# Kernel optimization log

Measured on AMD Instinct MI355X. Metric: run time of the kernel, lower is better.

## Reference

```python
import jax, jax.numpy as jnp
import numpy as np
from jax import lax

B = 8
INPUT_DIM = 2048
N_ENC = 2
VOCAB = 32000
EMBED = 512
HIDDEN = 512
MAX_LEN = 32
TEMP = 1.0


def setup_inputs() -> dict:
    key = jax.random.key(0)
    ks = jax.random.split(key, 12)
    s = 0.02
    inp = {
        "x": jax.random.normal(ks[0], (B, INPUT_DIM), jnp.float32),
        # encoder: N_ENC tanh layers input_dim->input_dim (stacked), then linear input_dim->embed
        "enc_w": jax.random.normal(ks[1], (N_ENC, INPUT_DIM, INPUT_DIM), jnp.float32) * s,
        "enc_b": jnp.zeros((N_ENC, INPUT_DIM), jnp.float32),
        "out_w": jax.random.normal(ks[2], (EMBED, INPUT_DIM), jnp.float32) * s,  # nn.Linear weight [out,in]
        "out_b": jnp.zeros((EMBED,), jnp.float32),
        # embeddings.weight: [vocab, hidden]; hidden_to_output = its transpose
        "emb_out": jax.random.normal(ks[3], (VOCAB, HIDDEN), jnp.float32) * s,
        # RelaxedEmbedding weight: [vocab, embed]
        "emb_in": jax.random.normal(ks[4], (VOCAB, EMBED), jnp.float32) * s,
        "prev_hidden0": jnp.zeros((HIDDEN,), jnp.float32),  # nn.Parameter init zeros
        # torch GRUCell params: weight_ih [3H, E], weight_hh [3H, H], biases [3H]
        "w_ih": jax.random.normal(ks[5], (3 * HIDDEN, EMBED), jnp.float32) * s,
        "b_ih": jnp.zeros((3 * HIDDEN,), jnp.float32),
        "w_hh": jax.random.normal(ks[6], (3 * HIDDEN, HIDDEN), jnp.float32) * s,
        "b_hh": jnp.zeros((3 * HIDDEN,), jnp.float32),
        # pre-sampled gumbel noise, one per step: [T, B, V]
        "gumbel": jax.random.gumbel(ks[7], (MAX_LEN, B, VOCAB), jnp.float32),
    }
    return inp


def reference(x, enc_w, enc_b, out_w, out_b, emb_out, emb_in, prev_hidden0,
              w_ih, b_ih, w_hh, b_hh, gumbel):
    # encoder MLP
    h = x
    for i in range(N_ENC):
        h = jnp.tanh(h @ enc_w[i].T + enc_b[i])
    img_feats = h @ out_w.T + out_b  # [B, EMBED]

    h0 = jnp.broadcast_to(prev_hidden0, (x.shape[0], HIDDEN))
    e0 = jnp.zeros_like(img_feats)  # sos_embedding * img_feats == 0

    def step(carry, g_t):
        h_prev, e_t = carry
        gi = e_t @ w_ih.T + b_ih      # [B, 3H]
        gh = h_prev @ w_hh.T + b_hh   # [B, 3H]
        i_r, i_z, i_n = jnp.split(gi, 3, axis=-1)
        h_r, h_z, h_n = jnp.split(gh, 3, axis=-1)
        r = jax.nn.sigmoid(i_r + h_r)
        z = jax.nn.sigmoid(i_z + h_z)
        n = jnp.tanh(i_n + r * h_n)
        h_t = (1.0 - z) * n + z * h_prev               # GRUCell
        logits = h_t @ emb_out.T                        # [B, V]
        x_t = jax.nn.softmax((logits + g_t) / TEMP, axis=-1)  # relaxed one-hot (training, no ST)
        e_next = (x_t @ emb_in) * img_feats             # RelaxedEmbedding * img_feats
        return (h_t, e_next), x_t

    _, seq = lax.scan(step, (h0, e0), gumbel)  # [T, B, V]
    return jnp.transpose(seq, (1, 0, 2))        # [B, T, V]
```

## Files before the change

### kernel.cpp

```cpp
#include <hip/hip_runtime.h>
#include <math.h>

constexpr int DIM = 2048, EMB = 512, HID = 512, VOC = 32000, TLEN = 32, G3 = 1536;
constexpr int NB = 256;
constexpr int NT = 256;
constexpr int ROWS = 125;
constexpr unsigned MAGIC = 0x13579BDFu;

constexpr size_t W_H1  = 0;
constexpr size_t W_H2  = W_H1 + 8 * 2048;
constexpr size_t W_IMG = W_H2 + 8 * 2048;
constexpr size_t W_GI  = W_IMG + 8 * 512;
constexpr size_t W_GH  = W_GI + 8 * 1536;
constexpr size_t W_SB  = W_GH + 8 * 1536;
constexpr size_t W_RS  = W_SB + (size_t)TLEN * 4096;
constexpr size_t W_AF  = W_RS + TLEN * 8;
constexpr size_t W_GF  = W_AF + 256 * 16;
constexpr size_t W_HF  = W_GF + 64 * 16;
constexpr size_t W_CNT = W_HF + 64 * 16;
constexpr size_t W_RDY = W_CNT + 32;
constexpr int FLAG_WORDS = 256 * 16 + 64 * 16 * 2 + 32;

__device__ __forceinline__ float dot4(float4 a, float4 b) {
  return a.x * b.x + a.y * b.y + a.z * b.z + a.w * b.w;
}
__device__ __forceinline__ float4 fma4(float4 acc, float s, float4 v) {
  acc.x += s * v.x; acc.y += s * v.y; acc.z += s * v.z; acc.w += s * v.w; return acc;
}
__device__ __forceinline__ float4 add4(float4 a, float4 b) {
  a.x += b.x; a.y += b.y; a.z += b.z; a.w += b.w; return a;
}
__device__ __forceinline__ float sigm(float x) { return 1.0f / (1.0f + __expf(-x)); }
__device__ __forceinline__ float selLane8(const float pb[8]) {
  int lane = threadIdx.x & 63;
  float r = 0.0f;
#pragma unroll
  for (int b = 0; b < 8; b++) r = (lane == b) ? pb[b] : r;
  return r;
}

__device__ __forceinline__ void stC(float* p, float v) {
  __hip_atomic_store(p, v, __ATOMIC_RELAXED, __HIP_MEMORY_SCOPE_AGENT);
}
__device__ __forceinline__ float ldC(const float* p) {
  return __hip_atomic_load(p, __ATOMIC_RELAXED, __HIP_MEMORY_SCOPE_AGENT);
}
__device__ __forceinline__ void vdrain() {
  asm volatile("s_waitcnt vmcnt(0)" ::: "memory");
}

template <int KLEN>
__device__ __forceinline__ void rowdot8(const float* __restrict__ wrow,
                                        const float* __restrict__ xsrc, float pb[8]) {
  constexpr int PER = KLEN / 64;
  constexpr int NF4 = PER / 4;
  int lane = threadIdx.x & 63;
  int k0 = lane * PER;
  const float4* w4 = (const float4*)(wrow + k0);
  float4 wv[NF4];
#pragma unroll
  for (int i = 0; i < NF4; i++) wv[i] = w4[i];
#pragma unroll
  for (int b = 0; b < 8; b++) {
    const float4* x4 = (const float4*)(xsrc + b * KLEN + k0);
    float s = 0.0f;
#pragma unroll
    for (int i = 0; i < NF4; i++) s += dot4(x4[i], wv[i]);
    pb[b] = s;
  }
#pragma unroll
  for (int m = 1; m < 64; m <<= 1) {
#pragma unroll
    for (int b = 0; b < 8; b++) pb[b] += __shfl_xor(pb[b], m, 64);
  }
}

__device__ __forceinline__ void postSlotF(unsigned* slot, unsigned val) {
  __syncthreads();
  if (threadIdx.x == 0) {
    __threadfence();
    __hip_atomic_store(slot, val, __ATOMIC_RELEASE, __HIP_MEMORY_SCOPE_AGENT);
  }
}
__device__ __forceinline__ void pollSlotsF(const unsigned* slots, int n, unsigned tgt) {
  int tid = threadIdx.x;
  if (tid < n) {
    const unsigned* p = slots + (size_t)tid * 16;
    while (__hip_atomic_load(p, __ATOMIC_RELAXED, __HIP_MEMORY_SCOPE_AGENT) < tgt)
      __builtin_amdgcn_s_sleep(1);
  }
  __syncthreads();
  __threadfence();
}

__device__ __forceinline__ void postSlotQ(unsigned* slot, unsigned val) {
  vdrain();
  __syncthreads();
  if (threadIdx.x == 0)
    __hip_atomic_store(slot, val, __ATOMIC_RELAXED, __HIP_MEMORY_SCOPE_AGENT);
}
__device__ __forceinline__ void pollOne(const unsigned* p, unsigned tgt) {
  if (threadIdx.x == 0) {
    while (__hip_atomic_load(p, __ATOMIC_RELAXED, __HIP_MEMORY_SCOPE_AGENT) < tgt)
      __builtin_amdgcn_s_sleep(1);
  }
  __syncthreads();
}

__device__ __forceinline__ void vocabRow(int r, float4 a0, float4 a1, float4 i0, float4 i1,
                                         const float4 hf[8][2], float4 ea[8][2],
                                         float sums[8], float* __restrict__ p_lds,
                                         const float* __restrict__ gum_lds) {
  int lane = threadIdx.x & 63;
  float pb[8];
#pragma unroll
  for (int b = 0; b < 8; b++) pb[b] = dot4(hf[b][0], a0) + dot4(hf[b][1], a1);
#pragma unroll
  for (int m = 1; m < 64; m <<= 1) {
#pragma unroll
    for (int b = 0; b < 8; b++) pb[b] += __shfl_xor(pb[b], m, 64);
  }
#pragma unroll
  for (int b = 0; b < 8; b++) {
    pb[b] = __expf(pb[b] + gum_lds[r * 8 + b]);
    sums[b] += pb[b];
  }
  if (lane == 0) {
    *(float4*)&p_lds[r * 8] = make_float4(pb[0], pb[1], pb[2], pb[3]);
    *(float4*)&p_lds[r * 8 + 4] = make_float4(pb[4], pb[5], pb[6], pb[7]);
  }
#pragma unroll
  for (int b = 0; b < 8; b++) {
    ea[b][0] = fma4(ea[b][0], pb[b], i0);
    ea[b][1] = fma4(ea[b][1], pb[b], i1);
  }
}

__global__ void __launch_bounds__(NT, 1)
InformedRnnSenderFixedLengthGS_48704929136907_kernel(
    const float* __restrict__ x, const float* __restrict__ enc_w,
    const float* __restrict__ enc_b, const float* __restrict__ out_w,
    const float* __restrict__ out_b, const float* __restrict__ emb_out,
    const float* __restrict__ emb_in, const float* __restrict__ ph,
    const float* __restrict__ w_ih, const float* __restrict__ b_ih,
    const float* __restrict__ w_hh, const float* __restrict__ b_hh,
    const float* __restrict__ gum, float* __restrict__ out, float* __restrict__ ws) {
  const int tid = threadIdx.x, blk = blockIdx.x;
  const int lane = tid & 63, wave = tid >> 6;

  float* h1 = ws + W_H1;
  float* h2 = ws + W_H2;
  float* img = ws + W_IMG;
  float* giU = ws + W_GI;
  float* gh = ws + W_GH;
  float* sbufU = ws + W_SB;
  float* rs_acc = ws + W_RS;
  unsigned* aflag = (unsigned*)(ws + W_AF);
  unsigned* gflag = (unsigned*)(ws + W_GF);
  unsigned* hflag = (unsigned*)(ws + W_HF);
  unsigned* cnt_gru = (unsigned*)(ws + W_CNT);
  unsigned* cnt_e = (unsigned*)(ws + W_CNT) + 16;
  unsigned* ready = (unsigned*)(ws + W_RDY);

  __shared__ float h_lds[4096];
  __shared__ float red_e[4096];
  __shared__ float p_lds[ROWS * 8];
  __shared__ float gum_lds[ROWS * 8];
  __shared__ float bih_lds[G3];
  __shared__ float red_rs[32];
  __shared__ float inv_lds[8];

  if (blk == 0) {
    for (int i = tid; i < FLAG_WORDS; i += NT) aflag[i] = 0u;
    __syncthreads();
    if (tid == 0) {
      __threadfence();
      __hip_atomic_store(ready, MAGIC, __ATOMIC_RELEASE, __HIP_MEMORY_SCOPE_AGENT);
    }
  }
  if (tid == 0) {
    while (__hip_atomic_load(ready, __ATOMIC_ACQUIRE, __HIP_MEMORY_SCOPE_AGENT) != MAGIC)
      __builtin_amdgcn_s_sleep(1);
  }
  __syncthreads();
  __threadfence();

#pragma unroll
  for (int rr = 0; rr < 2; rr++) {
    int o = blk * 8 + wave * 2 + rr;
    float pb[8];
    rowdot8<2048>(enc_w + (size_t)o * DIM, x, pb);
    float eb = enc_b[o];
#pragma unroll
    for (int b = 0; b < 8; b++) pb[b] = tanhf(pb[b] + eb);
    float myv = selLane8(pb);
    if (lane < 8) h1[lane * DIM + o] = myv;
  }
  postSlotF(&aflag[blk * 16], 1u);
  pollSlotsF(aflag, 256, 1u);

#pragma unroll
  for (int rr = 0; rr < 2; rr++) {
    int o = blk * 8 + wave * 2 + rr;
    float pb[8];
    rowdot8<2048>(enc_w + (size_t)DIM * DIM + (size_t)o * DIM, h1, pb);
    float eb = enc_b[DIM + o];
#pragma unroll
    for (int b = 0; b < 8; b++) pb[b] = tanhf(pb[b] + eb);
    float myv = selLane8(pb);
    if (lane < 8) h2[lane * DIM + o] = myv;
  }
  postSlotF(&aflag[blk * 16], 2u);
  pollSlotsF(aflag, 256, 2u);

  if (blk < 64) {
#pragma unroll
    for (int rr = 0; rr < 2; rr++) {
      int o = blk * 8 + wave * 2 + rr;
      float pb[8];
      rowdot8<2048>(out_w + (size_t)o * DIM, h2, pb);
      float ob = out_b[o];
#pragma unroll
      for (int b = 0; b < 8; b++) pb[b] += ob;
      float myv = selLane8(pb);
      if (lane < 8) img[lane * EMB + o] = myv;
    }
  } else if (blk < 128) {
    int local = blk - 64;
    int kk = lane * 8;
    float4 p0 = *(const float4*)(ph + kk);
    float4 p1 = *(const float4*)(ph + kk + 4);
    for (int r = 0; r < 6; r++) {
      int j = local * 24 + wave * 6 + r;
      const float4* w4 = (const float4*)(w_hh + (size_t)j * HID + kk);
      float s = dot4(p0, w4[0]) + dot4(p1, w4[1]);
#pragma unroll
      for (int m = 1; m < 64; m <<= 1) s += __shfl_xor(s, m, 64);
      float val = s + b_hh[j];
      if (lane < 8) gh[lane * G3 + j] = val;
    }
  } else if (blk < 192) {
    int local = blk - 128;
    for (int r = 0; r < 6; r++) {
      int j = local * 24 + wave * 6 + r;
      if (lane < 8) giU[lane * G3 + j] = 0.0f;
    }
  }
  for (int i = tid; i < 4096; i += NT) h_lds[i] = ph[i & 511];
  for (int i = tid; i < G3; i += NT) bih_lds[i] = b_ih[i];
  if (tid < 8) inv_lds[tid] = 1.0f;
  __syncthreads();
  postSlotF(&aflag[blk * 16], 3u);
  pollSlotsF(aflag, 256, 3u);

  const int v0 = blk * ROWS;
  const int k0 = lane * 8;
  const int rbeg = (wave * ROWS) / 4, rend = ((wave + 1) * ROWS) / 4;

  for (int t = 0; t < TLEN; ++t) {
    for (int i = tid; i < ROWS * 8; i += NT) {
      int b = i / ROWS, vl = i - b * ROWS;
      gum_lds[vl * 8 + b] = gum[(size_t)t * (8 * VOC) + (size_t)b * VOC + v0 + vl];
    }
    if (t > 0) {
      if (tid < 64) {
        const unsigned* p = gflag + (size_t)tid * 16;
        while (__hip_atomic_load(p, __ATOMIC_RELAXED, __HIP_MEMORY_SCOPE_AGENT) < (unsigned)t)
          __builtin_amdgcn_s_sleep(1);
      } else if (tid < 128) {
        const unsigned* p = hflag + (size_t)(tid - 64) * 16;
        while (__hip_atomic_load(p, __ATOMIC_RELAXED, __HIP_MEMORY_SCOPE_AGENT) < (unsigned)t)
          __builtin_amdgcn_s_sleep(1);
      }
      __syncthreads();
    }
#pragma unroll
    for (int qq = 0; qq < 4; qq++) {
      int i4 = tid + NT * qq;
      int b = i4 >> 7, k = (i4 & 127) * 4;
      float invb = inv_lds[b];
      const float* gib = giU + b * G3 + k;
      const float* ghb = gh + b * G3 + k;
      float4 iru, izu, inu, hrv, hzv, hnv;
      iru.x = ldC(gib + 0); iru.y = ldC(gib + 1); iru.z = ldC(gib + 2); iru.w = ldC(gib + 3);
      izu.x = ldC(gib + 512); izu.y = ldC(gib + 513); izu.z = ldC(gib + 514); izu.w = ldC(gib + 515);
      inu.x = ldC(gib + 1024); inu.y = ldC(gib + 1025); inu.z = ldC(gib + 1026); inu.w = ldC(gib + 1027);
      hrv.x = ldC(ghb + 0); hrv.y = ldC(ghb + 1); hrv.z = ldC(ghb + 2); hrv.w = ldC(ghb + 3);
      hzv.x = ldC(ghb + 512); hzv.y = ldC(ghb + 513); hzv.z = ldC(ghb + 514); hzv.w = ldC(ghb + 515);
      hnv.x = ldC(ghb + 1024); hnv.y = ldC(ghb + 1025); hnv.z = ldC(ghb + 1026); hnv.w = ldC(ghb + 1027);
      float4 br = *(const float4*)&bih_lds[k];
      float4 bz = *(const float4*)&bih_lds[512 + k];
      float4 bn = *(const float4*)&bih_lds[1024 + k];
      float4 hp = *(const float4*)&h_lds[b * 512 + k];
      float4 hv;
      {
        float r0 = sigm(invb * iru.x + br.x + hrv.x), z0 = sigm(invb * izu.x + bz.x + hzv.x);
        float n0 = tanhf(invb * inu.x + bn.x + r0 * hnv.x);
        hv.x = (1.0f - z0) * n0 + z0 * hp.x;
        r0 = sigm(invb * iru.y + br.y + hrv.y); z0 = sigm(invb * izu.y + bz.y + hzv.y);
        n0 = tanhf(invb * inu.y + bn.y + r0 * hnv.y);
        hv.y = (1.0f - z0) * n0 + z0 * hp.y;
        r0 = sigm(invb * iru.z + br.z + hrv.z); z0 = sigm(invb * izu.z + bz.z + hzv.z);
        n0 = tanhf(invb * inu.z + bn.z + r0 * hnv.z);
        hv.z = (1.0f - z0) * n0 + z0 * hp.z;
        r0 = sigm(invb * iru.w + br.w + hrv.w); z0 = sigm(invb * izu.w + bz.w + hzv.w);
        n0 = tanhf(invb * inu.w + bn.w + r0 * hnv.w);
        hv.w = (1.0f - z0) * n0 + z0 * hp.w;
      }
      *(float4*)&h_lds[b * 512 + k] = hv;
    }
    __syncthreads();
    if (tid == 0)
      __hip_atomic_fetch_add(cnt_gru, 1u, __ATOMIC_RELAXED, __HIP_MEMORY_SCOPE_AGENT);
    float4 hf[8][2];
#pragma unroll
    for (int b = 0; b < 8; b++) {
      hf[b][0] = *(const float4*)(h_lds + b * 512 + k0);
      hf[b][1] = *(const float4*)(h_lds + b * 512 + k0 + 4);
    }
    float4 ea[8][2];
#pragma unroll
    for (int b = 0; b < 8; b++) { ea[b][0] = make_float4(0, 0, 0, 0); ea[b][1] = make_float4(0, 0, 0, 0); }
    float sums[8] = {0, 0, 0, 0, 0, 0, 0, 0};
    int r = rbeg;
    for (; r + 8 <= rend; r += 8) {
      float4 A0[8], A1[8], I0[8], I1[8];
#pragma unroll
      for (int u = 0; u < 8; u++) {
        int v = v0 + r + u;
        const float4* wo = (const float4*)(emb_out + (size_t)v * EMB + k0);
        A0[u] = wo[0]; A1[u] = wo[1];
        const float4* wi = (const float4*)(emb_in + (size_t)v * EMB + k0);
        I0[u] = wi[0]; I1[u] = wi[1];
      }
#pragma unroll
      for (int u = 0; u < 8; u++)
        vocabRow(r + u, A0[u], A1[u], I0[u], I1[u], hf, ea, sums, p_lds, gum_lds);
    }
    {
      int rem = rend - r;
      if (rem > 0) {
        float4 A0[8], A1[8], I0[8], I1[8];
#pragma unroll
        for (int u = 0; u < 8; u++) {
          int rr = (u < rem) ? (r + u) : r;
          int v = v0 + rr;
          const float4* wo = (const float4*)(emb_out + (size_t)v * EMB + k0);
          A0[u] = wo[0]; A1[u] = wo[1];
          const float4* wi = (const float4*)(emb_in + (size_t)v * EMB + k0);
          I0[u] = wi[0]; I1[u] = wi[1];
        }
#pragma unroll
        for (int u = 0; u < 8; u++)
          if (u < rem)
            vocabRow(r + u, A0[u], A1[u], I0[u], I1[u], hf, ea, sums, p_lds, gum_lds);
      }
    }
    for (int w = 0; w < 4; w++) {
      if (wave == w) {
#pragma unroll
        for (int b = 0; b < 8; b++) {
          float4* d = (float4*)&red_e[b * 512 + k0];
          if (w == 0) { d[0] = ea[b][0]; d[1] = ea[b][1]; }
          else { d[0] = add4(d[0], ea[b][0]); d[1] = add4(d[1], ea[b][1]); }
        }
      }
      __syncthreads();
    }
    if (lane == 0) {
      *(float4*)&red_rs[wave * 8] = make_float4(sums[0], sums[1], sums[2], sums[3]);
      *(float4*)&red_rs[wave * 8 + 4] = make_float4(sums[4], sums[5], sums[6], sums[7]);
    }
    __syncthreads();
    {
      float* sb = sbufU + (size_t)t * 4096;
      for (int i = tid; i < 4096; i += NT) unsafeAtomicAdd(&sb[i], red_e[i]);
      if (tid < 8) {
        float tot = red_rs[tid] + red_rs[8 + tid] + red_rs[16 + tid] + red_rs[24 + tid];
        unsafeAtomicAdd(&rs_acc[t * 8 + tid], tot);
      }
    }
    vdrain();
    __syncthreads();
    if (tid == 0)
      __hip_atomic_fetch_add(cnt_e, 1u, __ATOMIC_RELAXED, __HIP_MEMORY_SCOPE_AGENT);

    if (blk >= 64 && blk < 128 && t < TLEN - 1) {
      pollOne(cnt_e, (unsigned)(NB * (t + 1)));
      float sf[8][8];
#pragma unroll
      for (int b = 0; b < 8; b++)
#pragma unroll
        for (int q = 0; q < 8; q++)
          sf[b][q] = ldC(sbufU + (size_t)t * 4096 + b * 512 + k0 + q) * img[b * 512 + k0 + q];
      int local = blk - 64;
      for (int r2 = 0; r2 < 6; r2++) {
        int j = local * 24 + wave * 6 + r2;
        const float* wr = w_ih + (size_t)j * HID + k0;
        float4 w0 = *(const float4*)wr, w1 = *(const float4*)(wr + 4);
        float wv[8] = {w0.x, w0.y, w0.z, w0.w, w1.x, w1.y, w1.z, w1.w};
        float pb[8];
#pragma unroll
        for (int b = 0; b < 8; b++) {
          float s = 0.0f;
#pragma unroll
          for (int q = 0; q < 8; q++) s += sf[b][q] * wv[q];
          pb[b] = s;
        }
#pragma unroll
        for (int m = 1; m < 64; m <<= 1) {
#pragma unroll
          for (int b = 0; b < 8; b++) pb[b] += __shfl_xor(pb[b], m, 64);
        }
        float myv = selLane8(pb);
        if (lane < 8) stC(&giU[lane * G3 + j], myv);
      }
      postSlotQ(&gflag[local * 16], (unsigned)(t + 1));
    }
    if (blk >= 128 && blk < 192 && t < TLEN - 1) {
      pollOne(cnt_gru, (unsigned)(NB * (t + 1)));
      int local = blk - 128;
      for (int r2 = 0; r2 < 6; r2++) {
        int j = local * 24 + wave * 6 + r2;
        const float4* w4 = (const float4*)(w_hh + (size_t)j * HID + k0);
        float4 w0 = w4[0], w1 = w4[1];
        float pb[8];
#pragma unroll
        for (int b = 0; b < 8; b++) pb[b] = dot4(hf[b][0], w0) + dot4(hf[b][1], w1);
#pragma unroll
        for (int m = 1; m < 64; m <<= 1) {
#pragma unroll
          for (int b = 0; b < 8; b++) pb[b] += __shfl_xor(pb[b], m, 64);
        }
        float bh = b_hh[j];
#pragma unroll
        for (int b = 0; b < 8; b++) pb[b] += bh;
        float myv = selLane8(pb);
        if (lane < 8) stC(&gh[lane * G3 + j], myv);
      }
      postSlotQ(&hflag[local * 16], (unsigned)(t + 1));
    }
    pollOne(cnt_e, (unsigned)(NB * (t + 1)));
    if (tid < 8) inv_lds[tid] = 1.0f / ldC(&rs_acc[t * 8 + tid]);
    __syncthreads();
    for (int i = tid; i < ROWS * 8; i += NT) {
      int b = i / ROWS, vl = i - b * ROWS;
      out[(size_t)b * ((size_t)TLEN * VOC) + (size_t)t * VOC + v0 + vl] =
          p_lds[vl * 8 + b] * inv_lds[b];
    }
  }
}

extern "C" void kernel_launch(void* const* d_in, const int* in_sizes, int n_in,
                              void* d_out, int out_size, void* d_ws, size_t ws_size,
                              hipStream_t stream) {
  const float* x = (const float*)d_in[0];
  const float* enc_w = (const float*)d_in[1];
  const float* enc_b = (const float*)d_in[2];
  const float* out_w = (const float*)d_in[3];
  const float* out_b = (const float*)d_in[4];
  const float* emb_out = (const float*)d_in[5];
  const float* emb_in = (const float*)d_in[6];
  const float* ph = (const float*)d_in[7];
  const float* w_ih = (const float*)d_in[8];
  const float* b_ih = (const float*)d_in[9];
  const float* w_hh = (const float*)d_in[10];
  const float* b_hh = (const float*)d_in[11];
  const float* gum = (const float*)d_in[12];
  float* out = (float*)d_out;
  float* ws = (float*)d_ws;

  InformedRnnSenderFixedLengthGS_48704929136907_kernel<<<dim3(NB), dim3(NT), 0, stream>>>(
      x, enc_w, enc_b, out_w, out_b, emb_out, emb_in, ph, w_ih, b_ih, w_hh, b_hh, gum,
      out, ws);
}
```

Measured before the change: 2.938 ms.

## Per-step gi/gh buffers; drop GRU barrier and compute gh before gi

Gives the gi and gh workspaces a separate slot for each timestep, so producers write step t+1 values without overwriting what other blocks still read for step t. This removes the cnt_gru global counter and its poll. The w_hh blocks now compute gh right after the step's atomics, before the gi blocks wait on cnt_e. The intent is to remove one grid-wide synchronization per step and shorten the critical path, at the cost of a larger workspace and reliance on the per-step buffering being correct.

```diff
diff --git a/kernel.cpp b/kernel.cpp
--- a/kernel.cpp
+++ b/kernel.cpp
@@ -5,21 +5,22 @@
 constexpr int NB = 256;
 constexpr int NT = 256;
 constexpr int ROWS = 125;
+constexpr int GSTEP = 12288;
 constexpr unsigned MAGIC = 0x13579BDFu;
 
 constexpr size_t W_H1  = 0;
-constexpr size_t W_H2  = W_H1 + 8 * 2048;
-constexpr size_t W_IMG = W_H2 + 8 * 2048;
-constexpr size_t W_GI  = W_IMG + 8 * 512;
-constexpr size_t W_GH  = W_GI + 8 * 1536;
-constexpr size_t W_SB  = W_GH + 8 * 1536;
+constexpr size_t W_H2  = W_H1 + 16384;
+constexpr size_t W_IMG = W_H2 + 16384;
+constexpr size_t W_GI  = W_IMG + 4096;
+constexpr size_t W_GH  = W_GI + 33 * (size_t)GSTEP;
+constexpr size_t W_SB  = W_GH + 33 * (size_t)GSTEP;
 constexpr size_t W_RS  = W_SB + (size_t)TLEN * 4096;
 constexpr size_t W_AF  = W_RS + TLEN * 8;
 constexpr size_t W_GF  = W_AF + 256 * 16;
 constexpr size_t W_HF  = W_GF + 64 * 16;
 constexpr size_t W_CNT = W_HF + 64 * 16;
-constexpr size_t W_RDY = W_CNT + 32;
-constexpr int FLAG_WORDS = 256 * 16 + 64 * 16 * 2 + 32;
+constexpr size_t W_RDY = W_CNT + 16;
+constexpr int FLAG_WORDS = 256 * 16 + 64 * 16 * 2 + 16;
 
 __device__ __forceinline__ float dot4(float4 a, float4 b) {
   return a.x * b.x + a.y * b.y + a.z * b.z + a.w * b.w;
@@ -105,6 +106,7 @@
       __builtin_amdgcn_s_sleep(1);
   }
   __syncthreads();
+  asm volatile("" ::: "memory");
 }
 
 __device__ __forceinline__ void vocabRow(int r, float4 a0, float4 a1, float4 i0, float4 i1,
@@ -158,8 +160,7 @@
   unsigned* aflag = (unsigned*)(ws + W_AF);
   unsigned* gflag = (unsigned*)(ws + W_GF);
   unsigned* hflag = (unsigned*)(ws + W_HF);
-  unsigned* cnt_gru = (unsigned*)(ws + W_CNT);
-  unsigned* cnt_e = (unsigned*)(ws + W_CNT) + 16;
+  unsigned* cnt_e = (unsigned*)(ws + W_CNT);
   unsigned* ready = (unsigned*)(ws + W_RDY);
 
   __shared__ float h_lds[4096];
@@ -273,45 +274,48 @@
           __builtin_amdgcn_s_sleep(1);
       }
       __syncthreads();
-    }
-#pragma unroll
-    for (int qq = 0; qq < 4; qq++) {
-      int i4 = tid + NT * qq;
-      int b = i4 >> 7, k = (i4 & 127) * 4;
-      float invb = inv_lds[b];
-      const float* gib = giU + b * G3 + k;
-      const float* ghb = gh + b * G3 + k;
-      float4 iru, izu, inu, hrv, hzv, hnv;
-      iru.x = ldC(gib + 0); iru.y = ldC(gib + 1); iru.z = ldC(gib + 2); iru.w = ldC(gib + 3);
-      izu.x = ldC(gib + 512); izu.y = ldC(gib + 513); izu.z = ldC(gib + 514); izu.w = ldC(gib + 515);
-      inu.x = ldC(gib + 1024); inu.y = ldC(gib + 1025); inu.z = ldC(gib + 1026); inu.w = ldC(gib + 1027);
-      hrv.x = ldC(ghb + 0); hrv.y = ldC(ghb + 1); hrv.z = ldC(ghb + 2); hrv.w = ldC(ghb + 3);
-      hzv.x = ldC(ghb + 512); hzv.y = ldC(ghb + 513); hzv.z = ldC(ghb + 514); hzv.w = ldC(ghb + 515);
-      hnv.x = ldC(ghb + 1024); hnv.y = ldC(ghb + 1025); hnv.z = ldC(ghb + 1026); hnv.w = ldC(ghb + 1027);
-      float4 br = *(const float4*)&bih_lds[k];
-      float4 bz = *(const float4*)&bih_lds[512 + k];
-      float4 bn = *(const float4*)&bih_lds[1024 + k];
-      float4 hp = *(const float4*)&h_lds[b * 512 + k];
-      float4 hv;
-      {
-        float r0 = sigm(invb * iru.x + br.x + hrv.x), z0 = sigm(invb * izu.x + bz.x + hzv.x);
-        float n0 = tanhf(invb * inu.x + bn.x + r0 * hnv.x);
-        hv.x = (1.0f - z0) * n0 + z0 * hp.x;
-        r0 = sigm(invb * iru.y + br.y + hrv.y); z0 = sigm(invb * izu.y + bz.y + hzv.y);
-        n0 = tanhf(invb * inu.y + bn.y + r0 * hnv.y);
-        hv.y = (1.0f - z0) * n0 + z0 * hp.y;
-        r0 = sigm(invb * iru.z + br.z + hrv.z); z0 = sigm(invb * izu.z + bz.z + hzv.z);
-        n0 = tanhf(invb * inu.z + bn.z + r0 * hnv.z);
-        hv.z = (1.0f - z0) * n0 + z0 * hp.z;
-        r0 = sigm(invb * iru.w + br.w + hrv.w); z0 = sigm(invb * izu.w + bz.w + hzv.w);
-        n0 = tanhf(invb * inu.w + bn.w + r0 * hnv.w);
-        hv.w = (1.0f - z0) * n0 + z0 * hp.w;
-      }
-      *(float4*)&h_lds[b * 512 + k] = hv;
+      asm volatile("" ::: "memory");
+    }
+    {
+      const float* giT = giU + (size_t)t * GSTEP;
+      const float* ghT = gh + (size_t)t * GSTEP;
+#pragma unroll
+      for (int qq = 0; qq < 4; qq++) {
+        int i4 = tid + NT * qq;
+        int b = i4 >> 7, k = (i4 & 127) * 4;
+        float invb = inv_lds[b];
+        const float* gib = giT + b * G3 + k;
+        const float* ghb = ghT + b * G3 + k;
+        float4 iru, izu, inu, hrv, hzv, hnv;
+        iru.x = ldC(gib + 0); iru.y = ldC(gib + 1); iru.z = ldC(gib + 2); iru.w = ldC(gib + 3);
+        izu.x = ldC(gib + 512); izu.y = ldC(gib + 513); izu.z = ldC(gib + 514); izu.w = ldC(gib + 515);
+        inu.x = ldC(gib + 1024); inu.y = ldC(gib + 1025); inu.z = ldC(gib + 1026); inu.w = ldC(gib + 1027);
+        hrv.x = ldC(ghb + 0); hrv.y = ldC(ghb + 1); hrv.z = ldC(ghb + 2); hrv.w = ldC(ghb + 3);
+        hzv.x = ldC(ghb + 512); hzv.y = ldC(ghb + 513); hzv.z = ldC(ghb + 514); hzv.w = ldC(ghb + 515);
+        hnv.x = ldC(ghb + 1024); hnv.y = ldC(ghb + 1025); hnv.z = ldC(ghb + 1026); hnv.w = ldC(ghb + 1027);
+        float4 br = *(const float4*)&bih_lds[k];
+        float4 bz = *(const float4*)&bih_lds[512 + k];
+        float4 bn = *(const float4*)&bih_lds[1024 + k];
+        float4 hp = *(const float4*)&h_lds[b * 512 + k];
+        float4 hv;
+        {
+          float r0 = sigm(invb * iru.x + br.x + hrv.x), z0 = sigm(invb * izu.x + bz.x + hzv.x);
+          float n0 = tanhf(invb * inu.x + bn.x + r0 * hnv.x);
+          hv.x = (1.0f - z0) * n0 + z0 * hp.x;
+          r0 = sigm(invb * iru.y + br.y + hrv.y); z0 = sigm(invb * izu.y + bz.y + hzv.y);
+          n0 = tanhf(invb * inu.y + bn.y + r0 * hnv.y);
+          hv.y = (1.0f - z0) * n0 + z0 * hp.y;
+          r0 = sigm(invb * iru.z + br.z + hrv.z); z0 = sigm(invb * izu.z + bz.z + hzv.z);
+          n0 = tanhf(invb * inu.z + bn.z + r0 * hnv.z);
+          hv.z = (1.0f - z0) * n0 + z0 * hp.z;
+          r0 = sigm(invb * iru.w + br.w + hrv.w); z0 = sigm(invb * izu.w + bz.w + hzv.w);
+          n0 = tanhf(invb * inu.w + bn.w + r0 * hnv.w);
+          hv.w = (1.0f - z0) * n0 + z0 * hp.w;
+        }
+        *(float4*)&h_lds[b * 512 + k] = hv;
+      }
     }
     __syncthreads();
-    if (tid == 0)
-      __hip_atomic_fetch_add(cnt_gru, 1u, __ATOMIC_RELAXED, __HIP_MEMORY_SCOPE_AGENT);
     float4 hf[8][2];
 #pragma unroll
     for (int b = 0; b < 8; b++) {
@@ -385,6 +389,29 @@
     if (tid == 0)
       __hip_atomic_fetch_add(cnt_e, 1u, __ATOMIC_RELAXED, __HIP_MEMORY_SCOPE_AGENT);
 
+    if (blk >= 128 && blk < 192 && t < TLEN - 1) {
+      float* ghN = gh + (size_t)(t + 1) * GSTEP;
+      int local = blk - 128;
+      for (int r2 = 0; r2 < 6; r2++) {
+        int j = local * 24 + wave * 6 + r2;
+        const float4* w4 = (const float4*)(w_hh + (size_t)j * HID + k0);
+        float4 w0 = w4[0], w1 = w4[1];
+        float pb[8];
+#pragma unroll
+        for (int b = 0; b < 8; b++) pb[b] = dot4(hf[b][0], w0) + dot4(hf[b][1], w1);
+#pragma unroll
+        for (int m = 1; m < 64; m <<= 1) {
+#pragma unroll
+          for (int b = 0; b < 8; b++) pb[b] += __shfl_xor(pb[b], m, 64);
+        }
+        float bh = b_hh[j];
+#pragma unroll
+        for (int b = 0; b < 8; b++) pb[b] += bh;
+        float myv = selLane8(pb);
+        if (lane < 8) stC(&ghN[lane * G3 + j], myv);
+      }
+      postSlotQ(&hflag[local * 16], (unsigned)(t + 1));
+    }
     if (blk >= 64 && blk < 128 && t < TLEN - 1) {
       pollOne(cnt_e, (unsigned)(NB * (t + 1)));
       float sf[8][8];
@@ -393,6 +420,7 @@
 #pragma unroll
         for (int q = 0; q < 8; q++)
           sf[b][q] = ldC(sbufU + (size_t)t * 4096 + b * 512 + k0 + q) * img[b * 512 + k0 + q];
+      float* giN = giU + (size_t)(t + 1) * GSTEP;
       int local = blk - 64;
       for (int r2 = 0; r2 < 6; r2++) {
         int j = local * 24 + wave * 6 + r2;
@@ -413,32 +441,9 @@
           for (int b = 0; b < 8; b++) pb[b] += __shfl_xor(pb[b], m, 64);
         }
         float myv = selLane8(pb);
-        if (lane < 8) stC(&giU[lane * G3 + j], myv);
+        if (lane < 8) stC(&giN[lane * G3 + j], myv);
       }
       postSlotQ(&gflag[local * 16], (unsigned)(t + 1));
-    }
-    if (blk >= 128 && blk < 192 && t < TLEN - 1) {
-      pollOne(cnt_gru, (unsigned)(NB * (t + 1)));
-      int local = blk - 128;
-      for (int r2 = 0; r2 < 6; r2++) {
-        int j = local * 24 + wave * 6 + r2;
-        const float4* w4 = (const float4*)(w_hh + (size_t)j * HID + k0);
-        float4 w0 = w4[0], w1 = w4[1];
-        float pb[8];
-#pragma unroll
-        for (int b = 0; b < 8; b++) pb[b] = dot4(hf[b][0], w0) + dot4(hf[b][1], w1);
-#pragma unroll
-        for (int m = 1; m < 64; m <<= 1) {
-#pragma unroll
-          for (int b = 0; b < 8; b++) pb[b] += __shfl_xor(pb[b], m, 64);
-        }
-        float bh = b_hh[j];
-#pragma unroll
-        for (int b = 0; b < 8; b++) pb[b] += bh;
-        float myv = selLane8(pb);
-        if (lane < 8) stC(&gh[lane * G3 + j], myv);
-      }
-      postSlotQ(&hflag[local * 16], (unsigned)(t + 1));
     }
     pollOne(cnt_e, (unsigned)(NB * (t + 1)));
     if (tid < 8) inv_lds[tid] = 1.0f / ldC(&rs_acc[t * 8 + tid]);
```

Result: faster. 2.717 ms (-7.5%).
